# Optimization experiments

Measured on AMD Instinct MI355X. Metric: run time of the kernel, lower is better.

The kernel has to match this reference:

```python
import jax, jax.numpy as jnp
import numpy as np

ALPHA = 0.2  # LeakyReLU negative slope
NEG_FILL = -9e15


def setup_inputs() -> dict:
    key = jax.random.key(0)
    k_adj, k_x, k_W, k_a = jax.random.split(key, 4)
    n, in_feats, out_feats = 12288, 256, 64
    adj = jax.random.randint(k_adj, (n, n), 0, 2, dtype=jnp.int32)
    x = jax.random.normal(k_x, (n, in_feats), dtype=jnp.float32)
    W = jax.random.normal(k_W, (in_feats, out_feats), dtype=jnp.float32) * 0.1
    a = jax.random.normal(k_a, (2 * out_feats, 1), dtype=jnp.float32) * 0.1
    return {"adj": adj, "x": x, "W": W, "a": a}


def reference(adj, x, W, a):
    out_feats = W.shape[1]
    h = x @ W                                  # (n, out_feats)
    wh1 = h @ a[:out_feats]                    # (n, 1)
    wh2 = h @ a[out_feats:]                    # (n, 1)
    e = jax.nn.leaky_relu(wh1 + wh2, ALPHA)    # (n, 1) -- faithful to source (no transpose)
    # broadcast (n,1) scores against (n,n) adjacency mask
    attention = jnp.where(adj > 0, e, NEG_FILL)
    attention = jax.nn.softmax(attention, axis=1)
    # dropout p=0.0 -> identity (eval mode)
    h_prime = attention @ h                    # (n, out_feats)
    return jax.nn.elu(h_prime)                 # concat=True
```

## Files before the change

kernel.cpp:

```cpp
#include <hip/hip_runtime.h>

#define N_NODES 12288
#define IN_F    256
#define OUT_F   64
#define KSPLIT  8
#define MT      64
#define KC      (N_NODES / KSPLIT)
#define STEPS   (KC / 32)
#define NSTRH   (N_NODES + 32)
#define NSTR8   (N_NODES + 64)

typedef __attribute__((ext_vector_type(8))) short bf16x8;
typedef __attribute__((ext_vector_type(4))) float f32x4;

__device__ __forceinline__ unsigned short f2bf(float f) {
    union { float f; unsigned int i; } v; v.f = f;
    unsigned int x = v.i;
    unsigned int r = x + 0x7FFFu + ((x >> 16) & 1u);
    return (unsigned short)(r >> 16);
}

__global__ __launch_bounds__(256) void k_pack(const int* __restrict__ adj,
                                              unsigned char* __restrict__ adj8) {
    const int row = blockIdx.x;
    const int t   = threadIdx.x;
    const int4* src = (const int4*)(adj + (size_t)row * N_NODES);
    unsigned int* dst = (unsigned int*)(adj8 + (size_t)row * NSTR8);
    #pragma unroll
    for (int j = 0; j < (N_NODES / 4) / 256; ++j) {
        int i = t + 256 * j;
        int4 a = src[i];
        dst[i] = (unsigned)a.x | ((unsigned)a.y << 8) |
                 ((unsigned)a.z << 16) | ((unsigned)a.w << 24);
    }
}

__global__ __launch_bounds__(256) void k_hT(const float* __restrict__ x,
                                            const float* __restrict__ W,
                                            unsigned short* __restrict__ hT) {
    __shared__ unsigned short WT[OUT_F][IN_F + 8];
    int tid = threadIdx.x;
    for (int idx = tid; idx < IN_F * OUT_F; idx += 256) {
        int k = idx >> 6, n = idx & 63;
        WT[n][k] = f2bf(W[idx]);
    }
    __syncthreads();

    int lane = tid & 63, wave = tid >> 6;
    int q = lane >> 4, ml = lane & 15;
    int i0 = blockIdx.x * MT;
    int row = i0 + 16 * wave + ml;
    const float* xr = x + (size_t)row * IN_F + 8 * q;

    f32x4 acc[4];
    #pragma unroll
    for (int nt = 0; nt < 4; ++nt) acc[nt] = (f32x4){0.f, 0.f, 0.f, 0.f};

    #pragma unroll
    for (int kk = 0; kk < IN_F; kk += 32) {
        float4 x0 = *(const float4*)(xr + kk);
        float4 x1 = *(const float4*)(xr + kk + 4);
        union { bf16x8 v; unsigned short u[8]; } A;
        A.u[0] = f2bf(x0.x); A.u[1] = f2bf(x0.y); A.u[2] = f2bf(x0.z); A.u[3] = f2bf(x0.w);
        A.u[4] = f2bf(x1.x); A.u[5] = f2bf(x1.y); A.u[6] = f2bf(x1.z); A.u[7] = f2bf(x1.w);
        #pragma unroll
        for (int nt = 0; nt < 4; ++nt) {
            bf16x8 bv = *(const bf16x8*)&WT[16 * nt + ml][kk + 8 * q];
            acc[nt] = __builtin_amdgcn_mfma_f32_16x16x32_bf16(A.v, bv, acc[nt], 0, 0, 0);
        }
    }

    #pragma unroll
    for (int nt = 0; nt < 4; ++nt) {
        ushort4 o;
        o.x = f2bf(acc[nt][0]); o.y = f2bf(acc[nt][1]);
        o.z = f2bf(acc[nt][2]); o.w = f2bf(acc[nt][3]);
        *(ushort4*)&hT[(size_t)(16 * nt + ml) * NSTRH + i0 + 16 * wave + 4 * q] = o;
    }
}

__global__ __launch_bounds__(256) void k_spmm(const unsigned char* __restrict__ adj8,
                                              const unsigned short* __restrict__ hT,
                                              float* __restrict__ s_part,
                                              float* __restrict__ deg_part) {
    const int tid  = threadIdx.x;
    const int lane = tid & 63;
    const int wave = tid >> 6;
    const int q    = lane >> 4;
    const int ml   = lane & 15;
    const int i0   = blockIdx.x * MT;
    const int ks   = blockIdx.y;
    const int k0   = ks * KC;
    const int row  = i0 + 16 * wave + ml;

    const unsigned char*  ap = adj8 + (size_t)row * NSTR8 + k0 + 8 * q;
    const unsigned short* bp = hT + (size_t)ml * NSTRH + k0 + 8 * q;

    union { bf16x8 v; unsigned short u[8]; } ones;
    #pragma unroll
    for (int i = 0; i < 8; ++i) ones.u[i] = 0x3F80;

    f32x4 acc[4], accd;
    #pragma unroll
    for (int nt = 0; nt < 4; ++nt) acc[nt] = (f32x4){0.f, 0.f, 0.f, 0.f};
    accd = (f32x4){0.f, 0.f, 0.f, 0.f};

#define LOADS(s, AA, B0, B1, B2, B3) do {                                      \
    AA = *(const uint2*)(ap + 32 * (size_t)(s));                               \
    const unsigned short* bq = bp + 32 * (s);                                  \
    B0 = *(const uint4*)(bq);                                                  \
    B1 = *(const uint4*)(bq + (size_t)16 * NSTRH);                             \
    B2 = *(const uint4*)(bq + (size_t)32 * NSTRH);                             \
    B3 = *(const uint4*)(bq + (size_t)48 * NSTRH);                             \
} while (0)

#define COMP(AA, B0, B1, B2, B3) do {                                          \
    unsigned int u_ = AA.x, v_ = AA.y;                                         \
    union { bf16x8 v; unsigned int w[4]; } av_;                                \
    av_.w[0] = ((u_ & 0xFFu)         | ((u_ & 0xFF00u) << 8)) * 0x3F80u;       \
    av_.w[1] = (((u_ >> 16) & 0xFFu) | ((u_ >> 24) << 16))    * 0x3F80u;       \
    av_.w[2] = ((v_ & 0xFFu)         | ((v_ & 0xFF00u) << 8)) * 0x3F80u;       \
    av_.w[3] = (((v_ >> 16) & 0xFFu) | ((v_ >> 24) << 16))    * 0x3F80u;       \
    acc[0] = __builtin_amdgcn_mfma_f32_16x16x32_bf16(av_.v, *(const bf16x8*)&B0, acc[0], 0, 0, 0); \
    acc[1] = __builtin_amdgcn_mfma_f32_16x16x32_bf16(av_.v, *(const bf16x8*)&B1, acc[1], 0, 0, 0); \
    acc[2] = __builtin_amdgcn_mfma_f32_16x16x32_bf16(av_.v, *(const bf16x8*)&B2, acc[2], 0, 0, 0); \
    acc[3] = __builtin_amdgcn_mfma_f32_16x16x32_bf16(av_.v, *(const bf16x8*)&B3, acc[3], 0, 0, 0); \
    accd   = __builtin_amdgcn_mfma_f32_16x16x32_bf16(av_.v, ones.v,              accd,   0, 0, 0); \
} while (0)

    uint2 aA, aB;
    uint4 b0A, b1A, b2A, b3A;
    uint4 b0B, b1B, b2B, b3B;

    LOADS(0, aA, b0A, b1A, b2A, b3A);
    for (int s = 0; s < STEPS - 2; s += 2) {
        LOADS(s + 1, aB, b0B, b1B, b2B, b3B);
        COMP(aA, b0A, b1A, b2A, b3A);
        LOADS(s + 2, aA, b0A, b1A, b2A, b3A);
        COMP(aB, b0B, b1B, b2B, b3B);
    }
    LOADS(STEPS - 1, aB, b0B, b1B, b2B, b3B);
    COMP(aA, b0A, b1A, b2A, b3A);
    COMP(aB, b0B, b1B, b2B, b3B);

#undef LOADS
#undef COMP

    float* sp = s_part + (size_t)ks * ((size_t)N_NODES * OUT_F);
    #pragma unroll
    for (int nt = 0; nt < 4; ++nt) {
        #pragma unroll
        for (int rr = 0; rr < 4; ++rr) {
            int orow = i0 + 16 * wave + 4 * q + rr;
            int ocol = 16 * nt + ml;
            sp[(size_t)orow * OUT_F + ocol] = acc[nt][rr];
        }
    }

    if (ml == 0) {
        #pragma unroll
        for (int rr = 0; rr < 4; ++rr)
            deg_part[ks * N_NODES + i0 + 16 * wave + 4 * q + rr] = accd[rr];
    }
}

__global__ __launch_bounds__(256) void k_out(const float* __restrict__ s_part,
                                             const float* __restrict__ deg_part,
                                             float* __restrict__ out) {
    int idx = blockIdx.x * 256 + threadIdx.x;
    int i = idx >> 6;
    float s = 0.f, deg = 0.f;
    #pragma unroll
    for (int p = 0; p < KSPLIT; ++p) {
        s   += s_part[(size_t)p * ((size_t)N_NODES * OUT_F) + idx];
        deg += deg_part[p * N_NODES + i];
    }
    float v = (deg > 0.5f) ? (s / deg) : 0.f;
    out[idx] = (v > 0.f) ? v : expm1f(v);
}

extern "C" void kernel_launch(void* const* d_in, const int* in_sizes, int n_in,
                              void* d_out, int out_size, void* d_ws, size_t ws_size,
                              hipStream_t stream) {
    const int*   adj = (const int*)d_in[0];
    const float* x   = (const float*)d_in[1];
    const float* W   = (const float*)d_in[2];
    float* out = (float*)d_out;

    char* ws = (char*)d_ws;
    const size_t hT_bytes  = (size_t)OUT_F * NSTRH * 2;
    const size_t sp_bytes  = (size_t)KSPLIT * N_NODES * OUT_F * 4;
    const size_t dp_bytes  = (size_t)KSPLIT * N_NODES * 4;
    unsigned short* hT     = (unsigned short*)ws;
    float* s_part          = (float*)(ws + hT_bytes);
    float* deg_part        = (float*)(ws + hT_bytes + sp_bytes);
    unsigned char* adj8    = (unsigned char*)(ws + hT_bytes + sp_bytes + dp_bytes);

    k_pack<<<dim3(N_NODES),               dim3(256), 0, stream>>>(adj, adj8);
    k_hT  <<<dim3(N_NODES / MT),          dim3(256), 0, stream>>>(x, W, hT);
    k_spmm<<<dim3(N_NODES / MT, KSPLIT),  dim3(256), 0, stream>>>(adj8, hT, s_part, deg_part);
    k_out <<<dim3(N_NODES * OUT_F / 256), dim3(256), 0, stream>>>(s_part, deg_part, out);
}
```

Measured before the change: 961.2 us.

## Fuse adjacency packing into SpMM with LDS-staged coalesced tiles

Removes the separate int32-to-byte adjacency pack kernel and has the SpMM kernel read the int32 adjacency directly with coalesced 16-byte loads. It converts the values to bf16 in registers and stages them through shared memory, along with tiles of the transposed features. The MFMA loop then reads operands from LDS over 128-wide K blocks, with register prefetch of the next tile. This eliminates the intermediate byte-matrix write and reread, at the cost of extra LDS traffic and two barriers per step.

```diff
diff --git a/kernel.cpp b/kernel.cpp
--- a/kernel.cpp
+++ b/kernel.cpp
@@ -6,9 +6,10 @@
 #define KSPLIT  8
 #define MT      64
 #define KC      (N_NODES / KSPLIT)
-#define STEPS   (KC / 32)
+#define BK      128
+#define NSTEP   (KC / BK)
 #define NSTRH   (N_NODES + 32)
-#define NSTR8   (N_NODES + 64)
+#define LPAD    8
 
 typedef __attribute__((ext_vector_type(8))) short bf16x8;
 typedef __attribute__((ext_vector_type(4))) float f32x4;
@@ -18,21 +19,6 @@
     unsigned int x = v.i;
     unsigned int r = x + 0x7FFFu + ((x >> 16) & 1u);
     return (unsigned short)(r >> 16);
-}
-
-__global__ __launch_bounds__(256) void k_pack(const int* __restrict__ adj,
-                                              unsigned char* __restrict__ adj8) {
-    const int row = blockIdx.x;
-    const int t   = threadIdx.x;
-    const int4* src = (const int4*)(adj + (size_t)row * N_NODES);
-    unsigned int* dst = (unsigned int*)(adj8 + (size_t)row * NSTR8);
-    #pragma unroll
-    for (int j = 0; j < (N_NODES / 4) / 256; ++j) {
-        int i = t + 256 * j;
-        int4 a = src[i];
-        dst[i] = (unsigned)a.x | ((unsigned)a.y << 8) |
-                 ((unsigned)a.z << 16) | ((unsigned)a.w << 24);
-    }
 }
 
 __global__ __launch_bounds__(256) void k_hT(const float* __restrict__ x,
@@ -79,10 +65,13 @@
     }
 }
 
-__global__ __launch_bounds__(256) void k_spmm(const unsigned char* __restrict__ adj8,
+__global__ __launch_bounds__(256) void k_spmm(const int* __restrict__ adj,
                                               const unsigned short* __restrict__ hT,
                                               float* __restrict__ s_part,
                                               float* __restrict__ deg_part) {
+    __shared__ unsigned short As[MT][BK + LPAD];
+    __shared__ unsigned short Bs[OUT_F][BK + LPAD];
+
     const int tid  = threadIdx.x;
     const int lane = tid & 63;
     const int wave = tid >> 6;
@@ -91,10 +80,14 @@
     const int i0   = blockIdx.x * MT;
     const int ks   = blockIdx.y;
     const int k0   = ks * KC;
-    const int row  = i0 + 16 * wave + ml;
-
-    const unsigned char*  ap = adj8 + (size_t)row * NSTR8 + k0 + 8 * q;
-    const unsigned short* bp = hT + (size_t)ml * NSTRH + k0 + 8 * q;
+
+    const int ar  = tid >> 5;
+    const int ac4 = tid & 31;
+    const int* ap = adj + (size_t)(i0 + ar) * N_NODES + k0 + 4 * ac4;
+
+    const int br  = tid >> 4;
+    const int bc8 = (tid & 15) * 8;
+    const unsigned short* bp = hT + (size_t)br * NSTRH + k0 + bc8;
 
     union { bf16x8 v; unsigned short u[8]; } ones;
     #pragma unroll
@@ -105,46 +98,55 @@
     for (int nt = 0; nt < 4; ++nt) acc[nt] = (f32x4){0.f, 0.f, 0.f, 0.f};
     accd = (f32x4){0.f, 0.f, 0.f, 0.f};
 
-#define LOADS(s, AA, B0, B1, B2, B3) do {                                      \
-    AA = *(const uint2*)(ap + 32 * (size_t)(s));                               \
-    const unsigned short* bq = bp + 32 * (s);                                  \
-    B0 = *(const uint4*)(bq);                                                  \
-    B1 = *(const uint4*)(bq + (size_t)16 * NSTRH);                             \
-    B2 = *(const uint4*)(bq + (size_t)32 * NSTRH);                             \
-    B3 = *(const uint4*)(bq + (size_t)48 * NSTRH);                             \
+    int4  a[8];
+    uint4 b[4];
+
+#define LOADT(s) do {                                                          \
+    _Pragma("unroll")                                                          \
+    for (int j = 0; j < 8; ++j)                                                \
+        a[j] = *(const int4*)(ap + (size_t)8 * j * N_NODES + (s) * BK);        \
+    _Pragma("unroll")                                                          \
+    for (int j = 0; j < 4; ++j)                                                \
+        b[j] = *(const uint4*)(bp + (size_t)16 * j * NSTRH + (s) * BK);        \
 } while (0)
 
-#define COMP(AA, B0, B1, B2, B3) do {                                          \
-    unsigned int u_ = AA.x, v_ = AA.y;                                         \
-    union { bf16x8 v; unsigned int w[4]; } av_;                                \
-    av_.w[0] = ((u_ & 0xFFu)         | ((u_ & 0xFF00u) << 8)) * 0x3F80u;       \
-    av_.w[1] = (((u_ >> 16) & 0xFFu) | ((u_ >> 24) << 16))    * 0x3F80u;       \
-    av_.w[2] = ((v_ & 0xFFu)         | ((v_ & 0xFF00u) << 8)) * 0x3F80u;       \
-    av_.w[3] = (((v_ >> 16) & 0xFFu) | ((v_ >> 24) << 16))    * 0x3F80u;       \
-    acc[0] = __builtin_amdgcn_mfma_f32_16x16x32_bf16(av_.v, *(const bf16x8*)&B0, acc[0], 0, 0, 0); \
-    acc[1] = __builtin_amdgcn_mfma_f32_16x16x32_bf16(av_.v, *(const bf16x8*)&B1, acc[1], 0, 0, 0); \
-    acc[2] = __builtin_amdgcn_mfma_f32_16x16x32_bf16(av_.v, *(const bf16x8*)&B2, acc[2], 0, 0, 0); \
-    acc[3] = __builtin_amdgcn_mfma_f32_16x16x32_bf16(av_.v, *(const bf16x8*)&B3, acc[3], 0, 0, 0); \
-    accd   = __builtin_amdgcn_mfma_f32_16x16x32_bf16(av_.v, ones.v,              accd,   0, 0, 0); \
+#define WRITET() do {                                                          \
+    _Pragma("unroll")                                                          \
+    for (int j = 0; j < 8; ++j) {                                              \
+        unsigned int lo = ((unsigned int)a[j].x + ((unsigned int)a[j].y << 16)) * 0x3F80u; \
+        unsigned int hi = ((unsigned int)a[j].z + ((unsigned int)a[j].w << 16)) * 0x3F80u; \
+        unsigned int* d = (unsigned int*)&As[ar + 8 * j][4 * ac4];             \
+        d[0] = lo; d[1] = hi;                                                  \
+    }                                                                          \
+    _Pragma("unroll")                                                          \
+    for (int j = 0; j < 4; ++j)                                                \
+        *(uint4*)&Bs[br + 16 * j][bc8] = b[j];                                 \
 } while (0)
 
-    uint2 aA, aB;
-    uint4 b0A, b1A, b2A, b3A;
-    uint4 b0B, b1B, b2B, b3B;
-
-    LOADS(0, aA, b0A, b1A, b2A, b3A);
-    for (int s = 0; s < STEPS - 2; s += 2) {
-        LOADS(s + 1, aB, b0B, b1B, b2B, b3B);
-        COMP(aA, b0A, b1A, b2A, b3A);
-        LOADS(s + 2, aA, b0A, b1A, b2A, b3A);
-        COMP(aB, b0B, b1B, b2B, b3B);
-    }
-    LOADS(STEPS - 1, aB, b0B, b1B, b2B, b3B);
-    COMP(aA, b0A, b1A, b2A, b3A);
-    COMP(aB, b0B, b1B, b2B, b3B);
-
-#undef LOADS
-#undef COMP
+    LOADT(0);
+
+    for (int s = 0; s < NSTEP; ++s) {
+        WRITET();
+        __syncthreads();
+
+        if (s + 1 < NSTEP) LOADT(s + 1);
+
+        #pragma unroll
+        for (int kk = 0; kk < BK; kk += 32) {
+            bf16x8 av = *(const bf16x8*)&As[16 * wave + ml][kk + 8 * q];
+            #pragma unroll
+            for (int nt = 0; nt < 4; ++nt) {
+                bf16x8 bv = *(const bf16x8*)&Bs[16 * nt + ml][kk + 8 * q];
+                acc[nt] = __builtin_amdgcn_mfma_f32_16x16x32_bf16(av, bv, acc[nt], 0, 0, 0);
+            }
+            accd = __builtin_amdgcn_mfma_f32_16x16x32_bf16(av, ones.v, accd, 0, 0, 0);
+        }
+
+        __syncthreads();
+    }
+
+#undef LOADT
+#undef WRITET
 
     float* sp = s_part + (size_t)ks * ((size_t)N_NODES * OUT_F);
     #pragma unroll
@@ -190,14 +192,11 @@
     char* ws = (char*)d_ws;
     const size_t hT_bytes  = (size_t)OUT_F * NSTRH * 2;
     const size_t sp_bytes  = (size_t)KSPLIT * N_NODES * OUT_F * 4;
-    const size_t dp_bytes  = (size_t)KSPLIT * N_NODES * 4;
     unsigned short* hT     = (unsigned short*)ws;
     float* s_part          = (float*)(ws + hT_bytes);
     float* deg_part        = (float*)(ws + hT_bytes + sp_bytes);
-    unsigned char* adj8    = (unsigned char*)(ws + hT_bytes + sp_bytes + dp_bytes);
-
-    k_pack<<<dim3(N_NODES),               dim3(256), 0, stream>>>(adj, adj8);
+
     k_hT  <<<dim3(N_NODES / MT),          dim3(256), 0, stream>>>(x, W, hT);
-    k_spmm<<<dim3(N_NODES / MT, KSPLIT),  dim3(256), 0, stream>>>(adj8, hT, s_part, deg_part);
+    k_spmm<<<dim3(N_NODES / MT, KSPLIT),  dim3(256), 0, stream>>>(adj, hT, s_part, deg_part);
     k_out <<<dim3(N_NODES * OUT_F / 256), dim3(256), 0, stream>>>(s_part, deg_part, out);
 }
```

After: 833.7 us. 1.15x faster.
